# Optimization experiments

Hardware: AMD Instinct MI355X
Metric: run time of the kernel (lower is better)

## Reference

```python
import jax, jax.numpy as jnp
import numpy as np

N = 4096      # number of nodes
C = 8         # channels (w1..w8 in source)
IN_DIM = 256  # input feature dim
D = 64        # per-channel dim (c_dim)
OUT = 128     # out_dim
ITERS = 4     # routing iterations
BETA = 1.0    # temperature
DENSITY = 0.01


def _l2norm(x):
    # tf.nn.l2_normalize along last axis with eps=1e-12
    return x * jax.lax.rsqrt(jnp.maximum(jnp.sum(x * x, axis=-1, keepdims=True), 1e-12))


def setup_inputs() -> dict:
    key = jax.random.key(0)
    k0, k1, k2, k3, k4, k5 = jax.random.split(key, 6)
    features = jax.random.normal(k0, (N, IN_DIM), dtype=jnp.float32)
    # sparse-ish 0/1 adjacency stored densely (as in the original model)
    adj = (jax.random.uniform(k1, (N, N)) < DENSITY).astype(jnp.float32)
    W = jax.random.normal(k2, (C, IN_DIM, D), dtype=jnp.float32)    # w1..w8 stacked
    b = jax.random.normal(k3, (C, 1, D), dtype=jnp.float32)         # b1..b8 stacked
    W_o = jax.random.normal(k4, (C * D, OUT), dtype=jnp.float32)
    bias = jax.random.normal(k5, (1, OUT), dtype=jnp.float32)
    return {"features": features, "adj": adj, "W": W, "b": b, "W_o": W_o, "bias": bias}


def reference(features, adj, W, b, W_o, bias):
    mask = adj > 0  # [N, N]
    # per-channel projection + l2 normalize: z[c] = l2norm(features @ w[c] + b[c])
    z = _l2norm(jnp.einsum('ni,cid->cnd', features, W) + b)  # [C, N, D]
    for _ in range(ITERS):
        # dense per-channel attention (XX^T), masked by adjacency
        A = jnp.einsum('cnd,cmd->cnm', z, z)                 # [C, N, N]
        A = jnp.where(mask[None], A, 0.0) / BETA
        # softmax across channels at each (i, j), then re-mask
        A = jax.nn.softmax(A, axis=0)
        A = jnp.where(mask[None], A, 0.0)
        # aggregate + residual + l2 normalize
        z = _l2norm(z + jnp.einsum('cnm,cmd->cnd', A, z))
    # concat channels along feature axis: [N, C*D]
    h = jnp.transpose(z, (1, 0, 2)).reshape(N, C * D)
    # (dropout skipped: stochastic op, identity in the deterministic reference)
    return h @ W_o + bias
```

## Files before the change

### kernel.cpp

```cpp
#include <hip/hip_runtime.h>
#include <hip/hip_bf16.h>

#define N_NODES 4096
#define C_CH    8
#define IN_DIM  256
#define D_DIM   64
#define CD      512
#define OUT_DIM 128
#define ITERS   4
#define STRIDE  128

typedef __hip_bfloat16 bf16;
typedef short short8 __attribute__((ext_vector_type(8)));
typedef float floatx4 __attribute__((ext_vector_type(4)));
typedef float v2f __attribute__((ext_vector_type(2)));

__device__ __forceinline__ float bf2f(bf16 x) { return __bfloat162float(x); }

__device__ __forceinline__ unsigned f2b_rne(float x) {
    unsigned u = __float_as_uint(x);
    return (u + 0x7FFFu + ((u >> 16) & 1u)) >> 16;
}
__device__ __forceinline__ unsigned pack2bf(float a, float b) {
    return f2b_rne(a) | (f2b_rne(b) << 16);
}
__device__ __forceinline__ void unpack2(unsigned v, float& a, float& b) {
    a = __uint_as_float(v << 16);
    b = __uint_as_float(v & 0xFFFF0000u);
}
__device__ __forceinline__ v2f unpack2v(unsigned v) {
    v2f r;
    r.x = __uint_as_float(v << 16);
    r.y = __uint_as_float(v & 0xFFFF0000u);
    return r;
}
__device__ __forceinline__ v2f fma2(v2f a, v2f b, v2f c) {
#if __has_builtin(__builtin_elementwise_fma)
    return __builtin_elementwise_fma(a, b, c);
#else
    v2f r; r.x = fmaf(a.x, b.x, c.x); r.y = fmaf(a.y, b.y, c.y); return r;
#endif
}
__device__ __forceinline__ short8 as_s8(uint4 u) {
    union { uint4 a; short8 b; } x; x.a = u; return x.b;
}

__device__ __forceinline__ bool wave_detect(const unsigned* __restrict__ feat_u) {
    int lane = threadIdx.x & 63;
    unsigned u = feat_u[lane];
    int e = (u >> 7) & 0xFF;
    int vote = (e >= 0x68 && e <= 0x86) ? 1 : 0;
    #pragma unroll
    for (int off = 32; off; off >>= 1) vote += __shfl_xor(vote, off);
    return vote >= 32;
}

__global__ __launch_bounds__(256) void stage_a(
        const void* __restrict__ feat, const void* __restrict__ W,
        const void* __restrict__ Wo,
        unsigned short* __restrict__ Wt, unsigned short* __restrict__ Wo_t) {
    bool isbf = wave_detect((const unsigned*)feat);
    int bx = blockIdx.x, t = threadIdx.x;
    if (bx < 8) {
        __shared__ __align__(16) unsigned short lt[IN_DIM * D_DIM];
        int c = bx;
        if (isbf) {
            const uint4* p = (const uint4*)((const unsigned short*)W + (size_t)c * IN_DIM * D_DIM);
            #pragma unroll
            for (int i = 0; i < 8; i++) {
                int idx = t + i * 256;
                *(uint4*)&lt[idx * 8] = p[idx];
            }
        } else {
            const float4* p = (const float4*)((const float*)W + (size_t)c * IN_DIM * D_DIM);
            #pragma unroll
            for (int i = 0; i < 16; i++) {
                int idx = t + i * 256;
                float4 f = p[idx];
                uint2 v = make_uint2(pack2bf(f.x, f.y), pack2bf(f.z, f.w));
                *(uint2*)&lt[idx * 4] = v;
            }
        }
        __syncthreads();
        uint4* wt4 = (uint4*)Wt;
        #pragma unroll
        for (int i = 0; i < 8; i++) {
            int j = t + i * 256;
            int d = j >> 5, seg = j & 31;
            int k0 = seg * 8;
            unsigned short v[8];
            #pragma unroll
            for (int k = 0; k < 8; k++) v[k] = lt[(k0 + k) * D_DIM + d];
            uint4 o;
            o.x = v[0] | ((unsigned)v[1] << 16);
            o.y = v[2] | ((unsigned)v[3] << 16);
            o.z = v[4] | ((unsigned)v[5] << 16);
            o.w = v[6] | ((unsigned)v[7] << 16);
            wt4[(c * 64 + d) * 32 + seg] = o;
        }
    } else {
        int base = (bx - 8) * 1024 + t * 4;
        #pragma unroll
        for (int q = 0; q < 4; q++) {
            int idx = base + q;
            int k = idx >> 7, n = idx & 127;
            unsigned short v;
            if (isbf) v = ((const unsigned short*)Wo)[idx];
            else      v = (unsigned short)f2b_rne(((const float*)Wo)[idx]);
            Wo_t[n * CD + k] = v;
        }
    }
}

__global__ __launch_bounds__(256) void stage_b(
        const void* __restrict__ feat, const void* __restrict__ adj,
        const void* __restrict__ b, const unsigned short* __restrict__ Wt,
        unsigned* __restrict__ zbf, int* __restrict__ deg,
        int* __restrict__ col_buf) {
    bool isbf = wave_detect((const unsigned*)feat);
    int bx = blockIdx.x, t = threadIdx.x;
    int w = t >> 6, lane = t & 63;
    __shared__ __align__(16) unsigned short zt[16 * CD];

    if (bx < 256) {
        int r0 = bx * 16;
        int n0 = w * 128;
        int m = lane & 15, quad = lane >> 4;
        int row = r0 + m;
        floatx4 acc[8];
        #pragma unroll
        for (int j = 0; j < 8; j++) acc[j] = (floatx4){0.f, 0.f, 0.f, 0.f};
        const uint4* wt4 = (const uint4*)Wt;

        if (isbf) {
            const uint4* a4 = (const uint4*)feat + (size_t)row * 32 + quad;
            #pragma unroll
            for (int k0 = 0; k0 < 8; k0++) {
                short8 a = as_s8(a4[k0 * 4]);
                #pragma unroll
                for (int j = 0; j < 8; j++) {
                    int col = n0 + j * 16 + m;
                    short8 bb = as_s8(wt4[col * 32 + k0 * 4 + quad]);
                    acc[j] = __builtin_amdgcn_mfma_f32_16x16x32_bf16(a, bb, acc[j], 0, 0, 0);
                }
            }
        } else {
            const float4* a4 = (const float4*)feat + (size_t)row * 64 + quad * 2;
            #pragma unroll
            for (int k0 = 0; k0 < 8; k0++) {
                float4 f0 = a4[k0 * 8], f1 = a4[k0 * 8 + 1];
                uint4 au;
                au.x = pack2bf(f0.x, f0.y); au.y = pack2bf(f0.z, f0.w);
                au.z = pack2bf(f1.x, f1.y); au.w = pack2bf(f1.z, f1.w);
                short8 a = as_s8(au);
                #pragma unroll
                for (int j = 0; j < 8; j++) {
                    int col = n0 + j * 16 + m;
                    short8 bb = as_s8(wt4[col * 32 + k0 * 4 + quad]);
                    acc[j] = __builtin_amdgcn_mfma_f32_16x16x32_bf16(a, bb, acc[j], 0, 0, 0);
                }
            }
        }

        float pre[8][4];
        #pragma unroll
        for (int j = 0; j < 8; j++) {
            int col = n0 + j * 16 + m;
            float bb = isbf ? bf2f(((const bf16*)b)[col]) : ((const float*)b)[col];
            #pragma unroll
            for (int r = 0; r < 4; r++) pre[j][r] = acc[j][r] + bb;
        }
        #pragma unroll
        for (int ch = 0; ch < 2; ch++) {
            float ss[4];
            #pragma unroll
            for (int r = 0; r < 4; r++) {
                float s = 0.f;
                #pragma unroll
                for (int jj = 0; jj < 4; jj++) {
                    float v = pre[ch * 4 + jj][r];
                    s = fmaf(v, v, s);
                }
                ss[r] = s;
            }
            #pragma unroll
            for (int off = 1; off < 16; off <<= 1) {
                #pragma unroll
                for (int r = 0; r < 4; r++) ss[r] += __shfl_xor(ss[r], off);
            }
            #pragma unroll
            for (int r = 0; r < 4; r++) {
                float sc = __builtin_amdgcn_rsqf(fmaxf(ss[r], 1e-12f));
                int lrow = quad * 4 + r;
                #pragma unroll
                for (int jj = 0; jj < 4; jj++) {
                    int j = ch * 4 + jj;
                    int col = n0 + j * 16 + m;
                    zt[lrow * CD + col] = (unsigned short)f2b_rne(pre[j][r] * sc);
                }
            }
        }
        __syncthreads();
        const uint4* zt4 = (const uint4*)zt;
        uint4* z4 = (uint4*)zbf;
        #pragma unroll
        for (int i = 0; i < 4; i++) {
            int j = t + i * 256;
            int lrow = j >> 6, seg = j & 63;
            z4[(size_t)(r0 + lrow) * 64 + seg] = zt4[j];
        }
    } else {
        int i = (bx - 256) * 4 + w;
        int base_out = i * STRIDE;
        int running = 0;
        int nch = isbf ? 8 : 16;
        for (int ch = 0; ch < nch; ch++) {
            unsigned bits = 0;
            int j0, nelem;
            if (isbf) {
                const uint4* p = (const uint4*)((const unsigned short*)adj + (size_t)i * N_NODES);
                uint4 u = p[ch * 64 + lane];
                j0 = (ch * 64 + lane) * 8; nelem = 8;
                unsigned short h[8] = {
                    (unsigned short)(u.x & 0xFFFF), (unsigned short)(u.x >> 16),
                    (unsigned short)(u.y & 0xFFFF), (unsigned short)(u.y >> 16),
                    (unsigned short)(u.z & 0xFFFF), (unsigned short)(u.z >> 16),
                    (unsigned short)(u.w & 0xFFFF), (unsigned short)(u.w >> 16)};
                #pragma unroll
                for (int k = 0; k < 8; k++)
                    if ((h[k] & 0x8000) == 0 && h[k] != 0) bits |= (1u << k);
            } else {
                const float4* p = (const float4*)((const float*)adj + (size_t)i * N_NODES);
                float4 f = p[ch * 64 + lane];
                j0 = (ch * 64 + lane) * 4; nelem = 4;
                if (f.x > 0.f) bits |= 1u;
                if (f.y > 0.f) bits |= 2u;
                if (f.z > 0.f) bits |= 4u;
                if (f.w > 0.f) bits |= 8u;
            }
            int cnt = __popc(bits);
            int sc = cnt;
            #pragma unroll
            for (int off = 1; off < 64; off <<= 1) {
                int v = __shfl_up(sc, off);
                if (lane >= off) sc += v;
            }
            int tot = __shfl(sc, 63);
            int pos = base_out + running + (sc - cnt);
            for (int k = 0; k < nelem; k++) {
                if ((bits >> k) & 1u) {
                    if (pos < base_out + STRIDE) col_buf[pos] = j0 + k;
                    pos++;
                }
            }
            running += tot;
        }
        if (lane == 0) deg[i] = (running < STRIDE) ? running : STRIDE;
    }
}

__device__ __forceinline__ void edge_step(const v2f zis[4], v2f acc[4], uint4 u,
                                          v2f vj[4]) {
    vj[0] = unpack2v(u.x);
    vj[1] = unpack2v(u.y);
    vj[2] = unpack2v(u.z);
    vj[3] = unpack2v(u.w);
    v2f p2 = zis[0] * vj[0];
    p2 = fma2(zis[1], vj[1], p2);
    p2 = fma2(zis[2], vj[2], p2);
    p2 = fma2(zis[3], vj[3], p2);
    float p = p2.x + p2.y;
    p += __shfl_xor(p, 1); p += __shfl_xor(p, 2); p += __shfl_xor(p, 4);
    float ex = exp2f(p);
    float s = ex;
    s += __shfl_xor(s, 8); s += __shfl_xor(s, 16); s += __shfl_xor(s, 32);
    float wgt = ex * __builtin_amdgcn_rcpf(s);
    v2f w2; w2.x = wgt; w2.y = wgt;
    acc[0] = fma2(w2, vj[0], acc[0]);
    acc[1] = fma2(w2, vj[1], acc[1]);
    acc[2] = fma2(w2, vj[2], acc[2]);
    acc[3] = fma2(w2, vj[3], acc[3]);
}

__global__ __launch_bounds__(256) void route_kernel(
        const unsigned* __restrict__ zbf_in, unsigned* __restrict__ zbf_out,
        const int* __restrict__ deg, const int* __restrict__ col_buf) {
    int t = threadIdx.x;
    int w = t >> 6, lane = t & 63;
    int i = blockIdx.x;
    int g = lane >> 3, s = lane & 7;
    __shared__ int   s_cols[STRIDE];
    __shared__ float s_acc[3][CD];
    if (t < STRIDE) s_cols[t] = col_buf[i * STRIDE + t];
    __syncthreads();

    int frag = g * 32 + s * 4;
    uint4 uown = *(const uint4*)(zbf_in + (size_t)i * 256 + frag);
    v2f z0[4], zis[4], acc[4];
    z0[0] = unpack2v(uown.x); z0[1] = unpack2v(uown.y);
    z0[2] = unpack2v(uown.z); z0[3] = unpack2v(uown.w);
    const float L2E = 1.44269504f;
    v2f l2e; l2e.x = L2E; l2e.y = L2E;
    #pragma unroll
    for (int k = 0; k < 4; k++) {
        zis[k] = z0[k] * l2e;
        if (w == 0) acc[k] = z0[k];
        else { acc[k].x = 0.f; acc[k].y = 0.f; }
    }

    int dg = deg[i];
    int e   = (dg * w) >> 2;
    int end = (dg * (w + 1)) >> 2;
    v2f vj[4];
    for (; e + 3 < end; e += 4) {
        int j0 = s_cols[e];
        int j1 = s_cols[e + 1];
        int j2 = s_cols[e + 2];
        int j3 = s_cols[e + 3];
        uint4 u0 = *(const uint4*)(zbf_in + (size_t)j0 * 256 + frag);
        uint4 u1 = *(const uint4*)(zbf_in + (size_t)j1 * 256 + frag);
        uint4 u2 = *(const uint4*)(zbf_in + (size_t)j2 * 256 + frag);
        uint4 u3 = *(const uint4*)(zbf_in + (size_t)j3 * 256 + frag);
        edge_step(zis, acc, u0, vj);
        edge_step(zis, acc, u1, vj);
        edge_step(zis, acc, u2, vj);
        edge_step(zis, acc, u3, vj);
    }
    for (; e < end; e++) {
        int j0 = s_cols[e];
        uint4 u0 = *(const uint4*)(zbf_in + (size_t)j0 * 256 + frag);
        edge_step(zis, acc, u0, vj);
    }

    int flat = g * D_DIM + s * 8;
    if (w) {
        *(float4*)&s_acc[w - 1][flat]     = make_float4(acc[0].x, acc[0].y, acc[1].x, acc[1].y);
        *(float4*)&s_acc[w - 1][flat + 4] = make_float4(acc[2].x, acc[2].y, acc[3].x, acc[3].y);
    }
    __syncthreads();
    if (w == 0) {
        #pragma unroll
        for (int q = 0; q < 3; q++) {
            float4 p0 = *(const float4*)&s_acc[q][flat];
            float4 p1 = *(const float4*)&s_acc[q][flat + 4];
            acc[0].x += p0.x; acc[0].y += p0.y; acc[1].x += p0.z; acc[1].y += p0.w;
            acc[2].x += p1.x; acc[2].y += p1.y; acc[3].x += p1.z; acc[3].y += p1.w;
        }
        v2f ss2 = acc[0] * acc[0];
        ss2 = fma2(acc[1], acc[1], ss2);
        ss2 = fma2(acc[2], acc[2], ss2);
        ss2 = fma2(acc[3], acc[3], ss2);
        float ss = ss2.x + ss2.y;
        ss += __shfl_xor(ss, 1); ss += __shfl_xor(ss, 2); ss += __shfl_xor(ss, 4);
        float sc = __builtin_amdgcn_rsqf(fmaxf(ss, 1e-12f));
        uint4 ob;
        ob.x = pack2bf(acc[0].x * sc, acc[0].y * sc);
        ob.y = pack2bf(acc[1].x * sc, acc[1].y * sc);
        ob.z = pack2bf(acc[2].x * sc, acc[2].y * sc);
        ob.w = pack2bf(acc[3].x * sc, acc[3].y * sc);
        *(uint4*)(zbf_out + (size_t)i * 256 + frag) = ob;
    }
}

__global__ __launch_bounds__(256) void out_gemm_mfma(
        const unsigned* __restrict__ zbf, const unsigned* __restrict__ wot_u,
        const void* __restrict__ bias, void* __restrict__ out,
        const void* __restrict__ feat) {
    bool isbf = wave_detect((const unsigned*)feat);
    int w = threadIdx.x >> 6, lane = threadIdx.x & 63;
    int r0 = blockIdx.x * 32 + (w & 1) * 16;
    int n0 = (w >> 1) * 64;
    int m = lane & 15, quad = lane >> 4;

    floatx4 acc0 = {0.f, 0.f, 0.f, 0.f}, acc1 = acc0, acc2 = acc0, acc3 = acc0;
    const unsigned* ap  = zbf   + (size_t)(r0 + m) * 256 + quad * 4;
    const unsigned* bp0 = wot_u + (size_t)(n0 + m) * 256 + quad * 4;
    const unsigned* bp1 = bp0 + 16 * 256;
    const unsigned* bp2 = bp0 + 32 * 256;
    const unsigned* bp3 = bp0 + 48 * 256;

    #pragma unroll
    for (int k0 = 0; k0 < 256; k0 += 16) {
        short8 a  = as_s8(*(const uint4*)(ap  + k0));
        short8 b0 = as_s8(*(const uint4*)(bp0 + k0));
        short8 b1 = as_s8(*(const uint4*)(bp1 + k0));
        short8 b2 = as_s8(*(const uint4*)(bp2 + k0));
        short8 b3 = as_s8(*(const uint4*)(bp3 + k0));
        acc0 = __builtin_amdgcn_mfma_f32_16x16x32_bf16(a, b0, acc0, 0, 0, 0);
        acc1 = __builtin_amdgcn_mfma_f32_16x16x32_bf16(a, b1, acc1, 0, 0, 0);
        acc2 = __builtin_amdgcn_mfma_f32_16x16x32_bf16(a, b2, acc2, 0, 0, 0);
        acc3 = __builtin_amdgcn_mfma_f32_16x16x32_bf16(a, b3, acc3, 0, 0, 0);
    }

    float accs[4][4] = {
        {acc0[0], acc0[1], acc0[2], acc0[3]},
        {acc1[0], acc1[1], acc1[2], acc1[3]},
        {acc2[0], acc2[1], acc2[2], acc2[3]},
        {acc3[0], acc3[1], acc3[2], acc3[3]}};
    #pragma unroll
    for (int c = 0; c < 4; c++) {
        int col = n0 + c * 16 + m;
        float bb = isbf ? bf2f(((const bf16*)bias)[col]) : ((const float*)bias)[col];
        #pragma unroll
        for (int r = 0; r < 4; r++) {
            int row = r0 + quad * 4 + r;
            float v = accs[c][r] + bb;
            size_t oi = (size_t)row * OUT_DIM + col;
            if (isbf) ((bf16*)out)[oi] = __float2bfloat16(v);
            else      ((float*)out)[oi] = v;
        }
    }
}

extern "C" void kernel_launch(void* const* d_in, const int* in_sizes, int n_in,
                              void* d_out, int out_size, void* d_ws, size_t ws_size,
                              hipStream_t stream) {
    const void* feat = d_in[0];
    const void* adj  = d_in[1];
    const void* W    = d_in[2];
    const void* b    = d_in[3];
    const void* Wo   = d_in[4];
    const void* bias = d_in[5];

    char* ws = (char*)d_ws;
    unsigned*       zbf_a   = (unsigned*)ws;
    unsigned*       zbf_b   = (unsigned*)(ws + (4u << 20));
    unsigned short* Wt      = (unsigned short*)(ws + (8u << 20));
    unsigned short* Wo_t    = (unsigned short*)(ws + (8u << 20) + (256u << 10));
    int*            deg     = (int*)(ws + (8u << 20) + (512u << 10));
    int*            col_buf = (int*)(ws + (9u << 20));

    stage_a<<<72, 256, 0, stream>>>(feat, W, Wo, Wt, Wo_t);
    stage_b<<<1280, 256, 0, stream>>>(feat, adj, b, Wt, zbf_a, deg, col_buf);

    unsigned* bin = zbf_a;
    unsigned* bot = zbf_b;
    for (int it = 0; it < ITERS; it++) {
        route_kernel<<<N_NODES, 256, 0, stream>>>(bin, bot, deg, col_buf);
        unsigned* tb = bin; bin = bot; bot = tb;
    }
    out_gemm_mfma<<<N_NODES / 32, 256, 0, stream>>>(zbf_a, (const unsigned*)Wo_t,
                                                    bias, d_out, feat);
}
```

Measured before the change: 224.1 us.

## Batch adjacency loads and register-shuffle neighbor indices in routing gather

The CSR-build branch now issues all row loads of the adjacency up front, in two batches of eight for fp32, before the scan and compaction, so memory latency overlaps. The route kernel drops the shared-memory column staging and its __syncthreads. Each wave instead loads its slice of neighbor indices into a lane register and broadcasts them with __shfl. The gather loop is unrolled to eight outstanding neighbor loads with a predicated tail, which adds memory-level parallelism at the cost of more live registers.

```diff
diff --git a/kernel.cpp b/kernel.cpp
--- a/kernel.cpp
+++ b/kernel.cpp
@@ -23,10 +23,6 @@
 }
 __device__ __forceinline__ unsigned pack2bf(float a, float b) {
     return f2b_rne(a) | (f2b_rne(b) << 16);
-}
-__device__ __forceinline__ void unpack2(unsigned v, float& a, float& b) {
-    a = __uint_as_float(v << 16);
-    b = __uint_as_float(v & 0xFFFF0000u);
 }
 __device__ __forceinline__ v2f unpack2v(unsigned v) {
     v2f r;
@@ -213,62 +209,85 @@
         int i = (bx - 256) * 4 + w;
         int base_out = i * STRIDE;
         int running = 0;
-        int nch = isbf ? 8 : 16;
-        for (int ch = 0; ch < nch; ch++) {
-            unsigned bits = 0;
-            int j0, nelem;
-            if (isbf) {
-                const uint4* p = (const uint4*)((const unsigned short*)adj + (size_t)i * N_NODES);
-                uint4 u = p[ch * 64 + lane];
-                j0 = (ch * 64 + lane) * 8; nelem = 8;
+        if (isbf) {
+            const uint4* p = (const uint4*)((const unsigned short*)adj + (size_t)i * N_NODES);
+            uint4 u[8];
+            #pragma unroll
+            for (int ch = 0; ch < 8; ch++) u[ch] = p[ch * 64 + lane];
+            #pragma unroll
+            for (int ch = 0; ch < 8; ch++) {
+                unsigned bits = 0;
+                int j0 = (ch * 64 + lane) * 8;
                 unsigned short h[8] = {
-                    (unsigned short)(u.x & 0xFFFF), (unsigned short)(u.x >> 16),
-                    (unsigned short)(u.y & 0xFFFF), (unsigned short)(u.y >> 16),
-                    (unsigned short)(u.z & 0xFFFF), (unsigned short)(u.z >> 16),
-                    (unsigned short)(u.w & 0xFFFF), (unsigned short)(u.w >> 16)};
+                    (unsigned short)(u[ch].x & 0xFFFF), (unsigned short)(u[ch].x >> 16),
+                    (unsigned short)(u[ch].y & 0xFFFF), (unsigned short)(u[ch].y >> 16),
+                    (unsigned short)(u[ch].z & 0xFFFF), (unsigned short)(u[ch].z >> 16),
+                    (unsigned short)(u[ch].w & 0xFFFF), (unsigned short)(u[ch].w >> 16)};
                 #pragma unroll
                 for (int k = 0; k < 8; k++)
                     if ((h[k] & 0x8000) == 0 && h[k] != 0) bits |= (1u << k);
-            } else {
-                const float4* p = (const float4*)((const float*)adj + (size_t)i * N_NODES);
-                float4 f = p[ch * 64 + lane];
-                j0 = (ch * 64 + lane) * 4; nelem = 4;
-                if (f.x > 0.f) bits |= 1u;
-                if (f.y > 0.f) bits |= 2u;
-                if (f.z > 0.f) bits |= 4u;
-                if (f.w > 0.f) bits |= 8u;
-            }
-            int cnt = __popc(bits);
-            int sc = cnt;
-            #pragma unroll
-            for (int off = 1; off < 64; off <<= 1) {
-                int v = __shfl_up(sc, off);
-                if (lane >= off) sc += v;
-            }
-            int tot = __shfl(sc, 63);
-            int pos = base_out + running + (sc - cnt);
-            for (int k = 0; k < nelem; k++) {
-                if ((bits >> k) & 1u) {
-                    if (pos < base_out + STRIDE) col_buf[pos] = j0 + k;
-                    pos++;
-                }
-            }
-            running += tot;
+                int cnt = __popc(bits);
+                int sc = cnt;
+                #pragma unroll
+                for (int off = 1; off < 64; off <<= 1) {
+                    int v = __shfl_up(sc, off);
+                    if (lane >= off) sc += v;
+                }
+                int tot = __shfl(sc, 63);
+                int pos = base_out + running + (sc - cnt);
+                for (int k = 0; k < 8; k++) {
+                    if ((bits >> k) & 1u) {
+                        if (pos < base_out + STRIDE) col_buf[pos] = j0 + k;
+                        pos++;
+                    }
+                }
+                running += tot;
+            }
+        } else {
+            const float4* p = (const float4*)((const float*)adj + (size_t)i * N_NODES);
+            #pragma unroll
+            for (int half = 0; half < 2; half++) {
+                float4 f[8];
+                #pragma unroll
+                for (int ch = 0; ch < 8; ch++) f[ch] = p[(half * 8 + ch) * 64 + lane];
+                #pragma unroll
+                for (int ch = 0; ch < 8; ch++) {
+                    unsigned bits = 0;
+                    int j0 = ((half * 8 + ch) * 64 + lane) * 4;
+                    if (f[ch].x > 0.f) bits |= 1u;
+                    if (f[ch].y > 0.f) bits |= 2u;
+                    if (f[ch].z > 0.f) bits |= 4u;
+                    if (f[ch].w > 0.f) bits |= 8u;
+                    int cnt = __popc(bits);
+                    int sc = cnt;
+                    #pragma unroll
+                    for (int off = 1; off < 64; off <<= 1) {
+                        int v = __shfl_up(sc, off);
+                        if (lane >= off) sc += v;
+                    }
+                    int tot = __shfl(sc, 63);
+                    int pos = base_out + running + (sc - cnt);
+                    for (int k = 0; k < 4; k++) {
+                        if ((bits >> k) & 1u) {
+                            if (pos < base_out + STRIDE) col_buf[pos] = j0 + k;
+                            pos++;
+                        }
+                    }
+                    running += tot;
+                }
+            }
         }
         if (lane == 0) deg[i] = (running < STRIDE) ? running : STRIDE;
     }
 }
 
-__device__ __forceinline__ void edge_step(const v2f zis[4], v2f acc[4], uint4 u,
-                                          v2f vj[4]) {
-    vj[0] = unpack2v(u.x);
-    vj[1] = unpack2v(u.y);
-    vj[2] = unpack2v(u.z);
-    vj[3] = unpack2v(u.w);
-    v2f p2 = zis[0] * vj[0];
-    p2 = fma2(zis[1], vj[1], p2);
-    p2 = fma2(zis[2], vj[2], p2);
-    p2 = fma2(zis[3], vj[3], p2);
+__device__ __forceinline__ void edge_step(const v2f zis[4], v2f acc[4], uint4 u) {
+    v2f vj0 = unpack2v(u.x), vj1 = unpack2v(u.y);
+    v2f vj2 = unpack2v(u.z), vj3 = unpack2v(u.w);
+    v2f p2 = zis[0] * vj0;
+    p2 = fma2(zis[1], vj1, p2);
+    p2 = fma2(zis[2], vj2, p2);
+    p2 = fma2(zis[3], vj3, p2);
     float p = p2.x + p2.y;
     p += __shfl_xor(p, 1); p += __shfl_xor(p, 2); p += __shfl_xor(p, 4);
     float ex = exp2f(p);
@@ -276,10 +295,10 @@
     s += __shfl_xor(s, 8); s += __shfl_xor(s, 16); s += __shfl_xor(s, 32);
     float wgt = ex * __builtin_amdgcn_rcpf(s);
     v2f w2; w2.x = wgt; w2.y = wgt;
-    acc[0] = fma2(w2, vj[0], acc[0]);
-    acc[1] = fma2(w2, vj[1], acc[1]);
-    acc[2] = fma2(w2, vj[2], acc[2]);
-    acc[3] = fma2(w2, vj[3], acc[3]);
+    acc[0] = fma2(w2, vj0, acc[0]);
+    acc[1] = fma2(w2, vj1, acc[1]);
+    acc[2] = fma2(w2, vj2, acc[2]);
+    acc[3] = fma2(w2, vj3, acc[3]);
 }
 
 __global__ __launch_bounds__(256) void route_kernel(
@@ -289,10 +308,12 @@
     int w = t >> 6, lane = t & 63;
     int i = blockIdx.x;
     int g = lane >> 3, s = lane & 7;
-    __shared__ int   s_cols[STRIDE];
     __shared__ float s_acc[3][CD];
-    if (t < STRIDE) s_cols[t] = col_buf[i * STRIDE + t];
-    __syncthreads();
+
+    int dg = deg[i];
+    int e0  = (dg * w) >> 2;
+    int cnt = ((dg * (w + 1)) >> 2) - e0;
+    int mycol = (lane < cnt) ? col_buf[i * STRIDE + e0 + lane] : 0;
 
     int frag = g * 32 + s * 4;
     uint4 uown = *(const uint4*)(zbf_in + (size_t)i * 256 + frag);
@@ -308,28 +329,25 @@
         else { acc[k].x = 0.f; acc[k].y = 0.f; }
     }
 
-    int dg = deg[i];
-    int e   = (dg * w) >> 2;
-    int end = (dg * (w + 1)) >> 2;
-    v2f vj[4];
-    for (; e + 3 < end; e += 4) {
-        int j0 = s_cols[e];
-        int j1 = s_cols[e + 1];
-        int j2 = s_cols[e + 2];
-        int j3 = s_cols[e + 3];
-        uint4 u0 = *(const uint4*)(zbf_in + (size_t)j0 * 256 + frag);
-        uint4 u1 = *(const uint4*)(zbf_in + (size_t)j1 * 256 + frag);
-        uint4 u2 = *(const uint4*)(zbf_in + (size_t)j2 * 256 + frag);
-        uint4 u3 = *(const uint4*)(zbf_in + (size_t)j3 * 256 + frag);
-        edge_step(zis, acc, u0, vj);
-        edge_step(zis, acc, u1, vj);
-        edge_step(zis, acc, u2, vj);
-        edge_step(zis, acc, u3, vj);
-    }
-    for (; e < end; e++) {
-        int j0 = s_cols[e];
-        uint4 u0 = *(const uint4*)(zbf_in + (size_t)j0 * 256 + frag);
-        edge_step(zis, acc, u0, vj);
+    for (int base = 0; base < cnt; base += 8) {
+        uint4 u0, u1, u2, u3, u4, u5, u6, u7;
+        int rem = cnt - base;
+        { int j = __shfl(mycol, base + 0);              u0 = *(const uint4*)(zbf_in + (size_t)j * 256 + frag); }
+        if (rem > 1) { int j = __shfl(mycol, base + 1); u1 = *(const uint4*)(zbf_in + (size_t)j * 256 + frag); }
+        if (rem > 2) { int j = __shfl(mycol, base + 2); u2 = *(const uint4*)(zbf_in + (size_t)j * 256 + frag); }
+        if (rem > 3) { int j = __shfl(mycol, base + 3); u3 = *(const uint4*)(zbf_in + (size_t)j * 256 + frag); }
+        if (rem > 4) { int j = __shfl(mycol, base + 4); u4 = *(const uint4*)(zbf_in + (size_t)j * 256 + frag); }
+        if (rem > 5) { int j = __shfl(mycol, base + 5); u5 = *(const uint4*)(zbf_in + (size_t)j * 256 + frag); }
+        if (rem > 6) { int j = __shfl(mycol, base + 6); u6 = *(const uint4*)(zbf_in + (size_t)j * 256 + frag); }
+        if (rem > 7) { int j = __shfl(mycol, base + 7); u7 = *(const uint4*)(zbf_in + (size_t)j * 256 + frag); }
+        edge_step(zis, acc, u0);
+        if (rem > 1) edge_step(zis, acc, u1);
+        if (rem > 2) edge_step(zis, acc, u2);
+        if (rem > 3) edge_step(zis, acc, u3);
+        if (rem > 4) edge_step(zis, acc, u4);
+        if (rem > 5) edge_step(zis, acc, u5);
+        if (rem > 6) edge_step(zis, acc, u6);
+        if (rem > 7) edge_step(zis, acc, u7);
     }
 
     int flat = g * D_DIM + s * 8;
```

New measurement: 227.8 us. Within noise of the previous version (+1.6%).
